# Kernel tuning notes

Measured on AMD Instinct MI355X. Metric: run time of the kernel, lower is better.

## Reference

```python
import jax, jax.numpy as jnp
import numpy as np

HEADS = 8
DIM_HEAD = 128
ATTN_MATRIX_SCALE = 1.5  # tau applied to mean-centered logits
SCALE = DIM_HEAD ** -0.5


def setup_inputs() -> dict:
    key = jax.random.key(0)
    ks = jax.random.split(key, 7)
    b, n, m = 2, 2048, 2048
    qd, cd, inner = 1024, 768, HEADS * DIM_HEAD
    x = jax.random.normal(ks[0], (b, n, qd), dtype=jnp.float32)
    context = jax.random.normal(ks[1], (b, m, cd), dtype=jnp.float32)
    Wq = jax.random.normal(ks[2], (qd, inner), dtype=jnp.float32) * (qd ** -0.5)
    Wk = jax.random.normal(ks[3], (cd, inner), dtype=jnp.float32) * (cd ** -0.5)
    Wv = jax.random.normal(ks[4], (cd, inner), dtype=jnp.float32) * (cd ** -0.5)
    Wout = jax.random.normal(ks[5], (inner, qd), dtype=jnp.float32) * (inner ** -0.5)
    bout = jnp.zeros((qd,), dtype=jnp.float32)
    return {"x": x, "context": context, "Wq": Wq, "Wk": Wk, "Wv": Wv,
            "Wout": Wout, "bout": bout}


def _split_heads(t):
    # (b, n, h*d) -> (h, b*n, d); matches rearrange '(b h) n d -> h (b n) d'
    b, n, _ = t.shape
    t = t.reshape(b, n, HEADS, DIM_HEAD)
    return t.transpose(2, 0, 1, 3).reshape(HEADS, b * n, DIM_HEAD)


def reference(x, context, Wq, Wk, Wv, Wout, bout):
    b, n, _ = x.shape
    qh = _split_heads(jnp.einsum('bnq,qi->bni', x, Wq))        # (h, b*n, d)
    kh = _split_heads(jnp.einsum('bmc,ci->bmi', context, Wk))  # (h, b*m, d)
    vh = _split_heads(jnp.einsum('bmc,ci->bmi', context, Wv))  # (h, b*m, d)

    # custom mean-centered / tau-scaled similarity (_compute_sim_with_tau)
    sim = jnp.einsum('hid,hjd->hij', qh, kh) * SCALE
    mean = jnp.mean(sim, axis=-1, keepdims=True)
    sim = (sim - mean) * ATTN_MATRIX_SCALE + mean

    attn = jax.nn.softmax(sim, axis=-1)
    out = jnp.einsum('hij,hjd->hid', attn, vh)                 # (h, b*n, d)

    # (h, b*n, d) -> (b, n, h*d)
    out = out.reshape(HEADS, b, n, DIM_HEAD).transpose(1, 2, 0, 3)
    out = out.reshape(b, n, HEADS * DIM_HEAD)
    return jnp.einsum('bni,iq->bnq', out, Wout) + bout
```

## Files before the change

kernel.cpp:

```cpp
#include <hip/hip_runtime.h>
#include <cstdint>
#include <cstddef>

typedef unsigned short u16t;
typedef __bf16 bf16x8_t __attribute__((ext_vector_type(8)));
typedef float f32x4_t __attribute__((ext_vector_type(4)));
typedef float f32x16_t __attribute__((ext_vector_type(16)));

#define MFMA_BF16 __builtin_amdgcn_mfma_f32_16x16x32_bf16
#define MFMA32    __builtin_amdgcn_mfma_f32_32x32x16_bf16

__device__ __forceinline__ u16t f2bf(float f) {
    uint32_t u = __builtin_bit_cast(uint32_t, f);
    u += 0x7fffu + ((u >> 16) & 1u);
    return (u16t)(u >> 16);
}

__device__ __forceinline__ uint32_t pk2bf(float a, float b) {
    return (uint32_t)f2bf(a) | ((uint32_t)f2bf(b) << 16);
}

__device__ __forceinline__ float bflo(uint32_t u) {
    return __builtin_bit_cast(float, u << 16);
}
__device__ __forceinline__ float bfhi(uint32_t u) {
    return __builtin_bit_cast(float, u & 0xffff0000u);
}

__device__ __forceinline__ bf16x8_t ld_frag(const u16t* p) {
    return __builtin_bit_cast(bf16x8_t, *(const uint4*)p);
}

__device__ __forceinline__ uint32_t cvtpk(float lo, float hi) {
    uint32_t r;
    asm("v_cvt_pk_bf16_f32 %0, %1, %2" : "=v"(r) : "v"(lo), "v"(hi));
    return r;
}
__device__ __forceinline__ void swap32(uint32_t& a, uint32_t& b) {
    asm("v_permlane32_swap_b32 %0, %1" : "+v"(a), "+v"(b));
}

__device__ __forceinline__ void gl_lds16(const u16t* g, u16t* l) {
    __builtin_amdgcn_global_load_lds(
        (const __attribute__((address_space(1))) void*)g,
        (__attribute__((address_space(3))) void*)l, 16, 0, 0);
}

__global__ void cast2_bf16_kernel(const float* __restrict__ s0, u16t* __restrict__ d0, int n0,
                                  const float* __restrict__ s1, u16t* __restrict__ d1, int n1) {
    int i = blockIdx.x * blockDim.x + threadIdx.x;
    const float* s; u16t* d;
    if (i < n0) { s = s0; d = d0; }
    else { i -= n0; if (i >= n1) return; s = s1; d = d1; }
    float4 v = ((const float4*)s)[i];
    uint2 o;
    o.x = pk2bf(v.x, v.y);
    o.y = pk2bf(v.z, v.w);
    ((uint2*)d)[i] = o;
}

__global__ void transpose4_kernel(const float* __restrict__ Wq, const float* __restrict__ Wk,
                                  const float* __restrict__ Wv, const float* __restrict__ Wo,
                                  u16t* __restrict__ Wqt, u16t* __restrict__ Wkt,
                                  u16t* __restrict__ Wvt, u16t* __restrict__ Wot) {
    const int z = blockIdx.z;
    const float* W = z == 0 ? Wq : (z == 1 ? Wk : (z == 2 ? Wv : Wo));
    u16t* Wt      = z == 0 ? Wqt : (z == 1 ? Wkt : (z == 2 ? Wvt : Wot));
    const int K   = (z == 1 || z == 2) ? 768 : 1024;
    const int N = 1024;
    int n0 = blockIdx.x * 32, k0 = blockIdx.y * 32;
    if (k0 >= K) return;
    __shared__ float tile[32][33];
    int tx = threadIdx.x, ty = threadIdx.y;
    for (int i = ty; i < 32; i += 8)
        tile[i][tx] = W[(size_t)(k0 + i) * N + n0 + tx];
    __syncthreads();
    for (int i = ty; i < 32; i += 8)
        Wt[(size_t)(n0 + i) * K + k0 + tx] = f2bf(tile[tx][i]);
}

__device__ __forceinline__ void gemm_core(
    const u16t* __restrict__ A, const u16t* __restrict__ Bt,
    int K, void* __restrict__ outp, const float* __restrict__ bias,
    int mode, float oscale, int bm, int bn)
{
    __shared__ __align__(16) u16t As[2][128 * 64];
    __shared__ __align__(16) u16t Bs[2][64 * 64];
    const int tid = threadIdx.x;
    const int wave = tid >> 6, lane = tid & 63;
    const int wm = wave & 1, wn = wave >> 1;
    const int quad = lane >> 4, l16 = lane & 15;

    const int l8r = lane >> 3, l8c = lane & 7;
    const int cgx = (l8c ^ l8r) * 8;

    f32x4_t acc[4][2];
#pragma unroll
    for (int i = 0; i < 4; ++i)
#pragma unroll
        for (int j = 0; j < 2; ++j) acc[i][j] = (f32x4_t){0.f, 0.f, 0.f, 0.f};

    const int nk = K >> 6;

#pragma unroll
    for (int it = 0; it < 4; ++it) {
        int rb = wave * 32 + it * 8;
        gl_lds16(&A[(size_t)(bm + rb + l8r) * K + cgx], &As[0][rb * 64]);
    }
#pragma unroll
    for (int it = 0; it < 2; ++it) {
        int rb = wave * 16 + it * 8;
        gl_lds16(&Bt[(size_t)(bn + rb + l8r) * K + cgx], &Bs[0][rb * 64]);
    }

    for (int ki = 0; ki < nk; ++ki) {
        const int buf = ki & 1;
        __syncthreads();

        if (ki + 1 < nk) {
            const int kc = (ki + 1) << 6;
#pragma unroll
            for (int it = 0; it < 4; ++it) {
                int rb = wave * 32 + it * 8;
                gl_lds16(&A[(size_t)(bm + rb + l8r) * K + kc + cgx], &As[buf ^ 1][rb * 64]);
            }
#pragma unroll
            for (int it = 0; it < 2; ++it) {
                int rb = wave * 16 + it * 8;
                gl_lds16(&Bt[(size_t)(bn + rb + l8r) * K + kc + cgx], &Bs[buf ^ 1][rb * 64]);
            }
        }

#pragma unroll
        for (int ks = 0; ks < 2; ++ks) {
            bf16x8_t af[4], bfv[2];
#pragma unroll
            for (int i = 0; i < 4; ++i) {
                int r = wm * 64 + i * 16 + l16;
                af[i] = ld_frag(&As[buf][r * 64 + (((ks * 4 + quad) ^ (r & 7)) * 8)]);
            }
#pragma unroll
            for (int j = 0; j < 2; ++j) {
                int r = wn * 32 + j * 16 + l16;
                bfv[j] = ld_frag(&Bs[buf][r * 64 + (((ks * 4 + quad) ^ (r & 7)) * 8)]);
            }
#pragma unroll
            for (int i = 0; i < 4; ++i)
#pragma unroll
                for (int j = 0; j < 2; ++j)
                    acc[i][j] = MFMA_BF16(af[i], bfv[j], acc[i][j], 0, 0, 0);
        }
    }

    if (mode == 3) {
        float* out = (float*)outp;
#pragma unroll
        for (int j = 0; j < 2; ++j) {
            int c = bn + wn * 32 + j * 16 + l16;
            float b = bias[c];
#pragma unroll
            for (int i = 0; i < 4; ++i) {
                int rb = bm + wm * 64 + i * 16 + quad * 4;
#pragma unroll
                for (int r = 0; r < 4; ++r)
                    out[(size_t)(rb + r) * 1024 + c] = acc[i][j][r] + b;
            }
        }
    } else if (mode == 2) {
        u16t* out = (u16t*)outp;
#pragma unroll
        for (int i = 0; i < 4; ++i)
#pragma unroll
            for (int j = 0; j < 2; ++j) {
                int rb = bm + wm * 64 + i * 16 + quad * 4;
                int c = bn + wn * 32 + j * 16 + l16;
                int h = c >> 7, d = c & 127;
                uint2 pk;
                pk.x = pk2bf(acc[i][j][0], acc[i][j][1]);
                pk.y = pk2bf(acc[i][j][2], acc[i][j][3]);
                *(uint2*)&out[((size_t)h * 128 + d) * 4096 + rb] = pk;
            }
    } else {
        u16t* out = (u16t*)outp;
#pragma unroll
        for (int i = 0; i < 4; ++i)
#pragma unroll
            for (int j = 0; j < 2; ++j) {
                int rb = bm + wm * 64 + i * 16 + quad * 4;
                int c = bn + wn * 32 + j * 16 + l16;
                int h = c >> 7, d = c & 127;
#pragma unroll
                for (int r = 0; r < 4; ++r)
                    out[((size_t)h * 4096 + rb + r) * 128 + d] = f2bf(acc[i][j][r] * oscale);
            }
    }
}

__global__ __launch_bounds__(256) void gemm_bf16_kernel(
    const u16t* __restrict__ A, const u16t* __restrict__ Bt,
    int K, void* __restrict__ outp, const float* __restrict__ bias,
    int mode, float oscale)
{
    gemm_core(A, Bt, K, outp, bias, mode, oscale, blockIdx.y * 128, blockIdx.x * 64);
}

__global__ __launch_bounds__(256) void qkv_kernel(
    const u16t* __restrict__ x_bf, const u16t* __restrict__ ctx_bf,
    const u16t* __restrict__ Wqt, const u16t* __restrict__ Wkt,
    const u16t* __restrict__ Wvt,
    u16t* __restrict__ Qh, u16t* __restrict__ Kh, u16t* __restrict__ Vt,
    float qscale)
{
    const int z = blockIdx.z;
    const u16t* A  = (z == 0) ? x_bf : ctx_bf;
    const u16t* Bt = (z == 0) ? Wqt : ((z == 1) ? Wkt : Wvt);
    void* outp     = (z == 0) ? (void*)Qh : ((z == 1) ? (void*)Kh : (void*)Vt);
    const int K    = (z == 0) ? 1024 : 768;
    const int mode = (z == 2) ? 2 : 0;
    const float sc = (z == 0) ? qscale : 1.0f;
    gemm_core(A, Bt, K, outp, nullptr, mode, sc, blockIdx.y * 128, blockIdx.x * 64);
}

__global__ __launch_bounds__(256, 2) void flash_kernel(
    const u16t* __restrict__ Qh, const u16t* __restrict__ Kh,
    const u16t* __restrict__ Vtg, u16t* __restrict__ Op0,
    u16t* __restrict__ Op1, float* __restrict__ lp)
{
    extern __shared__ __align__(16) u16t smem[];
    const int h = blockIdx.y;
    const int q0 = blockIdx.x * 128;
    const int z = blockIdx.z;
    const int tid = threadIdx.x;
    const int wave = tid >> 6, lane = tid & 63;
    const int l31 = lane & 31, hh = lane >> 5;
    const int NT = 64;

    const u16t* Kg = Kh + (size_t)h * 4096 * 128 + (size_t)z * 2048 * 128;
    const u16t* Vg = Vtg + (size_t)h * 128 * 4096 + z * 2048;

    {
        const u16t* Qg = Qh + ((size_t)h * 4096 + q0) * 128;
#pragma unroll
        for (int it = 0; it < 8; ++it) {
            int slot = it * 256 + tid;
            int r = slot >> 4, c = slot & 15;
            uint4 v = *(const uint4*)&Qg[(size_t)r * 128 + c * 8];
            *(uint4*)&smem[r * 128 + ((c ^ (r & 15)) * 8)] = v;
        }
    }
    __syncthreads();
    bf16x8_t qf[8];
    {
        int r = wave * 32 + l31;
#pragma unroll
        for (int s = 0; s < 8; ++s)
            qf[s] = ld_frag(&smem[r * 128 + (((s * 2 + hh) ^ (r & 15)) * 8)]);
    }
    __syncthreads();

    const bool kRole = wave < 2;
    const int wh = wave & 1;
    const int rK = lane >> 4, cK = lane & 15;
    const int rV = lane >> 2, cV = lane & 3;

    if (kRole) {
#pragma unroll
        for (int it = 0; it < 4; ++it) {
            int is = wh * 4 + it;
            int rowL = is * 4 + rK;
            gl_lds16(Kg + (size_t)rowL * 128 + ((cK ^ (rowL & 15)) * 8),
                     smem + is * 512);
        }
    } else {
#pragma unroll
        for (int it = 0; it < 4; ++it) {
            int is = wh * 4 + it;
            int rowL = is * 16 + rV;
            gl_lds16(Vg + (size_t)rowL * 4096 + ((cV ^ ((rowL >> 1) & 3)) * 8),
                     smem + 8192 + is * 512);
        }
    }

    f32x16_t Ow[4];
#pragma unroll
    for (int dg = 0; dg < 4; ++dg)
#pragma unroll
        for (int r = 0; r < 16; ++r) Ow[dg][r] = 0.f;

    float lsum = 0.f;
    const int swz = l31 & 15;
    bf16x8_t pf0, pf1;
    int v_rd = 2;
    int v_wr = 1;

    for (int t = 0; t <= NT; ++t) {
        __syncthreads();

        if (t + 1 < NT) {
            const int j0 = (t + 1) * 32;
            if (kRole) {
                u16t* kd = smem + ((t + 1) & 1) * 4096;
#pragma unroll
                for (int it = 0; it < 4; ++it) {
                    int is = wh * 4 + it;
                    int rowL = is * 4 + rK;
                    gl_lds16(Kg + (size_t)(j0 + rowL) * 128 + ((cK ^ (rowL & 15)) * 8),
                             kd + is * 512);
                }
            } else {
                u16t* vd = smem + 8192 + v_wr * 4096;
#pragma unroll
                for (int it = 0; it < 4; ++it) {
                    int is = wh * 4 + it;
                    int rowL = is * 16 + rV;
                    gl_lds16(Vg + (size_t)rowL * 4096 + j0 + ((cV ^ ((rowL >> 1) & 3)) * 8),
                             vd + is * 512);
                }
            }
        }

        if (t >= 1) {
            const u16t* vb = smem + 8192 + v_rd * 4096;
            __builtin_amdgcn_s_setprio(1);
#pragma unroll
            for (int dg = 0; dg < 4; ++dg) {
                int rv = dg * 32 + l31;
                int vsw = (rv >> 1) & 3;
                bf16x8_t v0 = ld_frag(&vb[rv * 32 + ((hh ^ vsw) * 8)]);
                bf16x8_t v1 = ld_frag(&vb[rv * 32 + (((2 + hh) ^ vsw) * 8)]);
                Ow[dg] = MFMA32(v0, pf0, Ow[dg], 0, 0, 0);
                Ow[dg] = MFMA32(v1, pf1, Ow[dg], 0, 0, 0);
            }
            __builtin_amdgcn_s_setprio(0);
        }

        if (t < NT) {
            const u16t* kb = smem + (t & 1) * 4096;
            f32x16_t Sa, Sb;
#pragma unroll
            for (int r = 0; r < 16; ++r) { Sa[r] = 0.f; Sb[r] = 0.f; }
            __builtin_amdgcn_s_setprio(1);
#pragma unroll
            for (int s = 0; s < 8; s += 2) {
                bf16x8_t k0 = ld_frag(&kb[l31 * 128 + (((s * 2 + hh) ^ swz) * 8)]);
                bf16x8_t k1 = ld_frag(&kb[l31 * 128 + ((((s + 1) * 2 + hh) ^ swz) * 8)]);
                Sa = MFMA32(k0, qf[s], Sa, 0, 0, 0);
                Sb = MFMA32(k1, qf[s + 1], Sb, 0, 0, 0);
            }
            __builtin_amdgcn_s_setprio(0);

            float p[16];
#pragma unroll
            for (int r = 0; r < 16; ++r)
                p[r] = __builtin_amdgcn_exp2f(Sa[r] + Sb[r]);
            lsum += ((((p[0] + p[1]) + (p[2] + p[3])) + ((p[4] + p[5]) + (p[6] + p[7])))
                  + (((p[8] + p[9]) + (p[10] + p[11])) + ((p[12] + p[13]) + (p[14] + p[15]))));

            uint32_t w0 = cvtpk(p[0], p[1]),   w2 = cvtpk(p[4], p[5]);
            uint32_t w1 = cvtpk(p[2], p[3]),   w3 = cvtpk(p[6], p[7]);
            swap32(w0, w2); swap32(w1, w3);
            uint32_t y0 = cvtpk(p[8], p[9]),   y2 = cvtpk(p[12], p[13]);
            uint32_t y1 = cvtpk(p[10], p[11]), y3 = cvtpk(p[14], p[15]);
            swap32(y0, y2); swap32(y1, y3);
            uint4 pw0; pw0.x = w0; pw0.y = w1; pw0.z = w2; pw0.w = w3;
            uint4 pw1; pw1.x = y0; pw1.y = y1; pw1.z = y2; pw1.w = y3;
            pf0 = __builtin_bit_cast(bf16x8_t, pw0);
            pf1 = __builtin_bit_cast(bf16x8_t, pw1);
        }

        v_rd = v_rd + 1 == 3 ? 0 : v_rd + 1;
        v_wr = v_wr + 1 == 3 ? 0 : v_wr + 1;
    }

    lsum += __shfl_xor(lsum, 32, 64);
    u16t* Op = z ? Op1 : Op0;
    size_t i = (size_t)(q0 + wave * 32 + l31);
    if (hh == 0) lp[z * 32768 + i * 8 + h] = lsum;
#pragma unroll
    for (int dg = 0; dg < 4; ++dg)
#pragma unroll
        for (int g = 0; g < 4; ++g) {
            uint2 pk;
            pk.x = pk2bf(Ow[dg][g * 4 + 0], Ow[dg][g * 4 + 1]);
            pk.y = pk2bf(Ow[dg][g * 4 + 2], Ow[dg][g * 4 + 3]);
            *(uint2*)&Op[i * 1024 + h * 128 + dg * 32 + g * 8 + hh * 4] = pk;
        }
}

__global__ __launch_bounds__(256) void combine_kernel(
    const u16t* __restrict__ O0, const u16t* __restrict__ O1,
    const float* __restrict__ lp, u16t* __restrict__ out)
{
    int t = blockIdx.x * blockDim.x + threadIdx.x;
    int e = t << 3;
    int i = e >> 10, h = (e >> 7) & 7;
    float inv = 1.f / (lp[i * 8 + h] + lp[32768 + i * 8 + h]);
    uint4 a = ((const uint4*)O0)[t];
    uint4 b = ((const uint4*)O1)[t];
    uint4 r;
    r.x = pk2bf((bflo(a.x) + bflo(b.x)) * inv, (bfhi(a.x) + bfhi(b.x)) * inv);
    r.y = pk2bf((bflo(a.y) + bflo(b.y)) * inv, (bfhi(a.y) + bfhi(b.y)) * inv);
    r.z = pk2bf((bflo(a.z) + bflo(b.z)) * inv, (bfhi(a.z) + bfhi(b.z)) * inv);
    r.w = pk2bf((bflo(a.w) + bflo(b.w)) * inv, (bfhi(a.w) + bfhi(b.w)) * inv);
    ((uint4*)out)[t] = r;
}

extern "C" void kernel_launch(void* const* d_in, const int* in_sizes, int n_in,
                              void* d_out, int out_size, void* d_ws, size_t ws_size,
                              hipStream_t stream)
{
    (void)in_sizes; (void)n_in; (void)out_size; (void)ws_size;
    const float* x    = (const float*)d_in[0];
    const float* ctx  = (const float*)d_in[1];
    const float* Wq   = (const float*)d_in[2];
    const float* Wk   = (const float*)d_in[3];
    const float* Wv   = (const float*)d_in[4];
    const float* Wout = (const float*)d_in[5];
    const float* bout = (const float*)d_in[6];
    float* out = (float*)d_out;

    u16t* ws = (u16t*)d_ws;
    u16t* x_bf   = ws;
    u16t* ctx_bf = x_bf + 4194304;
    u16t* Wqt    = ctx_bf + 3145728;
    u16t* Wkt    = Wqt + 1048576;
    u16t* Wvt    = Wkt + 786432;
    u16t* Woutt  = Wvt + 786432;
    u16t* Qh     = Woutt + 1048576;
    u16t* Kh     = Qh + 4194304;
    u16t* Vt     = Kh + 4194304;
    u16t* Oh   = x_bf;
    u16t* Ohp1 = ws + 4194304;
    float* lp  = (float*)(ws + 8388608);

    constexpr float QSCALE = 1.5f * 0.08838834764831845f * 1.4426950408889634f;

    (void)hipFuncSetAttribute((const void*)flash_kernel,
                              hipFuncAttributeMaxDynamicSharedMemorySize, 40960);

    cast2_bf16_kernel<<<7168, 256, 0, stream>>>(x, x_bf, 1048576, ctx, ctx_bf, 786432);
    transpose4_kernel<<<dim3(32, 32, 4), dim3(32, 8), 0, stream>>>(
        Wq, Wk, Wv, Wout, Wqt, Wkt, Wvt, Woutt);

    qkv_kernel<<<dim3(16, 32, 3), 256, 0, stream>>>(
        x_bf, ctx_bf, Wqt, Wkt, Wvt, Qh, Kh, Vt, QSCALE);

    flash_kernel<<<dim3(32, 8, 2), 256, 40960, stream>>>(Qh, Kh, Vt, Oh, Ohp1, lp);
    combine_kernel<<<2048, 256, 0, stream>>>(Oh, Ohp1, lp, Oh);

    gemm_bf16_kernel<<<dim3(16, 32), 256, 0, stream>>>(Oh, Woutt, 1024, out, bout, 3, 1.0f);
}
```

Baseline: 239.3 us.

## Load Q/K/V fragments directly from global into registers, dropping LDS staging

```diff
diff --git a/kernel.cpp b/kernel.cpp
--- a/kernel.cpp
+++ b/kernel.cpp
@@ -226,7 +226,6 @@
     const u16t* __restrict__ Vtg, u16t* __restrict__ Op0,
     u16t* __restrict__ Op1, float* __restrict__ lp)
 {
-    extern __shared__ __align__(16) u16t smem[];
     const int h = blockIdx.y;
     const int q0 = blockIdx.x * 128;
     const int z = blockIdx.z;
@@ -238,49 +237,21 @@
     const u16t* Kg = Kh + (size_t)h * 4096 * 128 + (size_t)z * 2048 * 128;
     const u16t* Vg = Vtg + (size_t)h * 128 * 4096 + z * 2048;
 
-    {
-        const u16t* Qg = Qh + ((size_t)h * 4096 + q0) * 128;
-#pragma unroll
-        for (int it = 0; it < 8; ++it) {
-            int slot = it * 256 + tid;
-            int r = slot >> 4, c = slot & 15;
-            uint4 v = *(const uint4*)&Qg[(size_t)r * 128 + c * 8];
-            *(uint4*)&smem[r * 128 + ((c ^ (r & 15)) * 8)] = v;
-        }
-    }
-    __syncthreads();
     bf16x8_t qf[8];
     {
-        int r = wave * 32 + l31;
-#pragma unroll
-        for (int s = 0; s < 8; ++s)
-            qf[s] = ld_frag(&smem[r * 128 + (((s * 2 + hh) ^ (r & 15)) * 8)]);
-    }
-    __syncthreads();
-
-    const bool kRole = wave < 2;
-    const int wh = wave & 1;
-    const int rK = lane >> 4, cK = lane & 15;
-    const int rV = lane >> 2, cV = lane & 3;
-
-    if (kRole) {
-#pragma unroll
-        for (int it = 0; it < 4; ++it) {
-            int is = wh * 4 + it;
-            int rowL = is * 4 + rK;
-            gl_lds16(Kg + (size_t)rowL * 128 + ((cK ^ (rowL & 15)) * 8),
-                     smem + is * 512);
-        }
-    } else {
-#pragma unroll
-        for (int it = 0; it < 4; ++it) {
-            int is = wh * 4 + it;
-            int rowL = is * 16 + rV;
-            gl_lds16(Vg + (size_t)rowL * 4096 + ((cV ^ ((rowL >> 1) & 3)) * 8),
-                     smem + 8192 + is * 512);
-        }
-    }
-
+        const u16t* Qr = Qh + ((size_t)h * 4096 + q0 + wave * 32 + l31) * 128 + hh * 8;
+#pragma unroll
+        for (int s = 0; s < 8; ++s) qf[s] = ld_frag(Qr + s * 16);
+    }
+
+    const u16t* Kr0 = Kg + (size_t)l31 * 128 + hh * 8;
+    const u16t* Vr0 = Vg + (size_t)l31 * 4096 + hh * 8;
+
+    bf16x8_t kf[8];
+#pragma unroll
+    for (int s = 0; s < 8; ++s) kf[s] = ld_frag(Kr0 + s * 16);
+
+    bf16x8_t vf0[4], vf1[4];
     f32x16_t Ow[4];
 #pragma unroll
     for (int dg = 0; dg < 4; ++dg)
@@ -288,88 +259,65 @@
         for (int r = 0; r < 16; ++r) Ow[dg][r] = 0.f;
 
     float lsum = 0.f;
-    const int swz = l31 & 15;
     bf16x8_t pf0, pf1;
-    int v_rd = 2;
-    int v_wr = 1;
-
-    for (int t = 0; t <= NT; ++t) {
-        __syncthreads();
+
+    for (int t = 0; t < NT; ++t) {
+        f32x16_t Sa, Sb;
+#pragma unroll
+        for (int r = 0; r < 16; ++r) { Sa[r] = 0.f; Sb[r] = 0.f; }
+        __builtin_amdgcn_s_setprio(1);
+#pragma unroll
+        for (int s = 0; s < 8; s += 2) {
+            Sa = MFMA32(kf[s], qf[s], Sa, 0, 0, 0);
+            Sb = MFMA32(kf[s + 1], qf[s + 1], Sb, 0, 0, 0);
+        }
+        if (t >= 1) {
+#pragma unroll
+            for (int dg = 0; dg < 4; ++dg) {
+                Ow[dg] = MFMA32(vf0[dg], pf0, Ow[dg], 0, 0, 0);
+                Ow[dg] = MFMA32(vf1[dg], pf1, Ow[dg], 0, 0, 0);
+            }
+        }
+        __builtin_amdgcn_s_setprio(0);
 
         if (t + 1 < NT) {
-            const int j0 = (t + 1) * 32;
-            if (kRole) {
-                u16t* kd = smem + ((t + 1) & 1) * 4096;
-#pragma unroll
-                for (int it = 0; it < 4; ++it) {
-                    int is = wh * 4 + it;
-                    int rowL = is * 4 + rK;
-                    gl_lds16(Kg + (size_t)(j0 + rowL) * 128 + ((cK ^ (rowL & 15)) * 8),
-                             kd + is * 512);
-                }
-            } else {
-                u16t* vd = smem + 8192 + v_wr * 4096;
-#pragma unroll
-                for (int it = 0; it < 4; ++it) {
-                    int is = wh * 4 + it;
-                    int rowL = is * 16 + rV;
-                    gl_lds16(Vg + (size_t)rowL * 4096 + j0 + ((cV ^ ((rowL >> 1) & 3)) * 8),
-                             vd + is * 512);
-                }
-            }
-        }
-
-        if (t >= 1) {
-            const u16t* vb = smem + 8192 + v_rd * 4096;
-            __builtin_amdgcn_s_setprio(1);
+            const u16t* Kr = Kr0 + (size_t)(t + 1) * 4096;
+#pragma unroll
+            for (int s = 0; s < 8; ++s) kf[s] = ld_frag(Kr + s * 16);
+        }
+        {
+            const u16t* Vr = Vr0 + t * 32;
 #pragma unroll
             for (int dg = 0; dg < 4; ++dg) {
-                int rv = dg * 32 + l31;
-                int vsw = (rv >> 1) & 3;
-                bf16x8_t v0 = ld_frag(&vb[rv * 32 + ((hh ^ vsw) * 8)]);
-                bf16x8_t v1 = ld_frag(&vb[rv * 32 + (((2 + hh) ^ vsw) * 8)]);
-                Ow[dg] = MFMA32(v0, pf0, Ow[dg], 0, 0, 0);
-                Ow[dg] = MFMA32(v1, pf1, Ow[dg], 0, 0, 0);
-            }
-            __builtin_amdgcn_s_setprio(0);
-        }
-
-        if (t < NT) {
-            const u16t* kb = smem + (t & 1) * 4096;
-            f32x16_t Sa, Sb;
-#pragma unroll
-            for (int r = 0; r < 16; ++r) { Sa[r] = 0.f; Sb[r] = 0.f; }
-            __builtin_amdgcn_s_setprio(1);
-#pragma unroll
-            for (int s = 0; s < 8; s += 2) {
-                bf16x8_t k0 = ld_frag(&kb[l31 * 128 + (((s * 2 + hh) ^ swz) * 8)]);
-                bf16x8_t k1 = ld_frag(&kb[l31 * 128 + ((((s + 1) * 2 + hh) ^ swz) * 8)]);
-                Sa = MFMA32(k0, qf[s], Sa, 0, 0, 0);
-                Sb = MFMA32(k1, qf[s + 1], Sb, 0, 0, 0);
-            }
-            __builtin_amdgcn_s_setprio(0);
-
-            float p[16];
-#pragma unroll
-            for (int r = 0; r < 16; ++r)
-                p[r] = __builtin_amdgcn_exp2f(Sa[r] + Sb[r]);
-            lsum += ((((p[0] + p[1]) + (p[2] + p[3])) + ((p[4] + p[5]) + (p[6] + p[7])))
-                  + (((p[8] + p[9]) + (p[10] + p[11])) + ((p[12] + p[13]) + (p[14] + p[15]))));
-
-            uint32_t w0 = cvtpk(p[0], p[1]),   w2 = cvtpk(p[4], p[5]);
-            uint32_t w1 = cvtpk(p[2], p[3]),   w3 = cvtpk(p[6], p[7]);
-            swap32(w0, w2); swap32(w1, w3);
-            uint32_t y0 = cvtpk(p[8], p[9]),   y2 = cvtpk(p[12], p[13]);
-            uint32_t y1 = cvtpk(p[10], p[11]), y3 = cvtpk(p[14], p[15]);
-            swap32(y0, y2); swap32(y1, y3);
-            uint4 pw0; pw0.x = w0; pw0.y = w1; pw0.z = w2; pw0.w = w3;
-            uint4 pw1; pw1.x = y0; pw1.y = y1; pw1.z = y2; pw1.w = y3;
-            pf0 = __builtin_bit_cast(bf16x8_t, pw0);
-            pf1 = __builtin_bit_cast(bf16x8_t, pw1);
-        }
-
-        v_rd = v_rd + 1 == 3 ? 0 : v_rd + 1;
-        v_wr = v_wr + 1 == 3 ? 0 : v_wr + 1;
+                const u16t* vrp = Vr + (size_t)dg * 32 * 4096;
+                vf0[dg] = ld_frag(vrp);
+                vf1[dg] = ld_frag(vrp + 16);
+            }
+        }
+
+        float p[16];
+#pragma unroll
+        for (int r = 0; r < 16; ++r)
+            p[r] = __builtin_amdgcn_exp2f(Sa[r] + Sb[r]);
+        lsum += ((((p[0] + p[1]) + (p[2] + p[3])) + ((p[4] + p[5]) + (p[6] + p[7])))
+              + (((p[8] + p[9]) + (p[10] + p[11])) + ((p[12] + p[13]) + (p[14] + p[15]))));
+
+        uint32_t w0 = cvtpk(p[0], p[1]),   w2 = cvtpk(p[4], p[5]);
+        uint32_t w1 = cvtpk(p[2], p[3]),   w3 = cvtpk(p[6], p[7]);
+        swap32(w0, w2); swap32(w1, w3);
+        uint32_t y0 = cvtpk(p[8], p[9]),   y2 = cvtpk(p[12], p[13]);
+        uint32_t y1 = cvtpk(p[10], p[11]), y3 = cvtpk(p[14], p[15]);
+        swap32(y0, y2); swap32(y1, y3);
+        uint4 pw0; pw0.x = w0; pw0.y = w1; pw0.z = w2; pw0.w = w3;
+        uint4 pw1; pw1.x = y0; pw1.y = y1; pw1.z = y2; pw1.w = y3;
+        pf0 = __builtin_bit_cast(bf16x8_t, pw0);
+        pf1 = __builtin_bit_cast(bf16x8_t, pw1);
+    }
+
+#pragma unroll
+    for (int dg = 0; dg < 4; ++dg) {
+        Ow[dg] = MFMA32(vf0[dg], pf0, Ow[dg], 0, 0, 0);
+        Ow[dg] = MFMA32(vf1[dg], pf1, Ow[dg], 0, 0, 0);
     }
 
     lsum += __shfl_xor(lsum, 32, 64);
@@ -435,9 +383,6 @@
 
     constexpr float QSCALE = 1.5f * 0.08838834764831845f * 1.4426950408889634f;
 
-    (void)hipFuncSetAttribute((const void*)flash_kernel,
-                              hipFuncAttributeMaxDynamicSharedMemorySize, 40960);
-
     cast2_bf16_kernel<<<7168, 256, 0, stream>>>(x, x_bf, 1048576, ctx, ctx_bf, 786432);
     transpose4_kernel<<<dim3(32, 32, 4), dim3(32, 8), 0, stream>>>(
         Wq, Wk, Wv, Wout, Wqt, Wkt, Wvt, Woutt);
@@ -445,7 +390,7 @@
     qkv_kernel<<<dim3(16, 32, 3), 256, 0, stream>>>(
         x_bf, ctx_bf, Wqt, Wkt, Wvt, Qh, Kh, Vt, QSCALE);
 
-    flash_kernel<<<dim3(32, 8, 2), 256, 40960, stream>>>(Qh, Kh, Vt, Oh, Ohp1, lp);
+    flash_kernel<<<dim3(32, 8, 2), 256, 0, stream>>>(Qh, Kh, Vt, Oh, Ohp1, lp);
     combine_kernel<<<2048, 256, 0, stream>>>(Oh, Ohp1, lp, Oh);
 
     gemm_bf16_kernel<<<dim3(16, 32), 256, 0, stream>>>(Oh, Woutt, 1024, out, bout, 3, 1.0f);
```

Result: slower. 392.5 us (+64.0%).

## Double KV tile to 64 keys and restructure flash pipeline buffers

Applied to the files above, without the earlier changes.

```diff
diff --git a/kernel.cpp b/kernel.cpp
--- a/kernel.cpp
+++ b/kernel.cpp
@@ -233,7 +233,7 @@
     const int tid = threadIdx.x;
     const int wave = tid >> 6, lane = tid & 63;
     const int l31 = lane & 31, hh = lane >> 5;
-    const int NT = 64;
+    const int NT = 32;
 
     const u16t* Kg = Kh + (size_t)h * 4096 * 128 + (size_t)z * 2048 * 128;
     const u16t* Vg = Vtg + (size_t)h * 128 * 4096 + z * 2048;
@@ -261,24 +261,16 @@
     const bool kRole = wave < 2;
     const int wh = wave & 1;
     const int rK = lane >> 4, cK = lane & 15;
-    const int rV = lane >> 2, cV = lane & 3;
+    const int rV = lane >> 3, cV = lane & 7;
 
     if (kRole) {
 #pragma unroll
-        for (int it = 0; it < 4; ++it) {
-            int is = wh * 4 + it;
+        for (int it = 0; it < 8; ++it) {
+            int is = wh * 8 + it;
             int rowL = is * 4 + rK;
             gl_lds16(Kg + (size_t)rowL * 128 + ((cK ^ (rowL & 15)) * 8),
                      smem + is * 512);
         }
-    } else {
-#pragma unroll
-        for (int it = 0; it < 4; ++it) {
-            int is = wh * 4 + it;
-            int rowL = is * 16 + rV;
-            gl_lds16(Vg + (size_t)rowL * 4096 + ((cV ^ ((rowL >> 1) & 3)) * 8),
-                     smem + 8192 + is * 512);
-        }
     }
 
     f32x16_t Ow[4];
@@ -288,88 +280,89 @@
         for (int r = 0; r < 16; ++r) Ow[dg][r] = 0.f;
 
     float lsum = 0.f;
-    const int swz = l31 & 15;
-    bf16x8_t pf0, pf1;
-    int v_rd = 2;
-    int v_wr = 1;
+    const int swzk = l31 & 15;
+    bf16x8_t pf[4];
 
     for (int t = 0; t <= NT; ++t) {
         __syncthreads();
 
-        if (t + 1 < NT) {
-            const int j0 = (t + 1) * 32;
-            if (kRole) {
-                u16t* kd = smem + ((t + 1) & 1) * 4096;
-#pragma unroll
-                for (int it = 0; it < 4; ++it) {
-                    int is = wh * 4 + it;
+        if (kRole) {
+            if (t + 1 < NT) {
+                const int j0 = (t + 1) * 64;
+                u16t* kd = smem + ((t + 1) & 1) * 8192;
+#pragma unroll
+                for (int it = 0; it < 8; ++it) {
+                    int is = wh * 8 + it;
                     int rowL = is * 4 + rK;
                     gl_lds16(Kg + (size_t)(j0 + rowL) * 128 + ((cK ^ (rowL & 15)) * 8),
                              kd + is * 512);
                 }
-            } else {
-                u16t* vd = smem + 8192 + v_wr * 4096;
-#pragma unroll
-                for (int it = 0; it < 4; ++it) {
-                    int is = wh * 4 + it;
-                    int rowL = is * 16 + rV;
-                    gl_lds16(Vg + (size_t)rowL * 4096 + j0 + ((cV ^ ((rowL >> 1) & 3)) * 8),
+            }
+        } else {
+            if (t < NT) {
+                const int j0 = t * 64;
+                u16t* vd = smem + 16384 + (t & 1) * 8192;
+#pragma unroll
+                for (int it = 0; it < 8; ++it) {
+                    int is = wh * 8 + it;
+                    int rowL = is * 8 + rV;
+                    gl_lds16(Vg + (size_t)rowL * 4096 + j0 + ((cV ^ ((rowL ^ (rowL >> 3)) & 7)) * 8),
                              vd + is * 512);
                 }
             }
         }
 
+        __builtin_amdgcn_s_setprio(1);
+        f32x16_t St0, St1;
+#pragma unroll
+        for (int r = 0; r < 16; ++r) { St0[r] = 0.f; St1[r] = 0.f; }
+        if (t < NT) {
+            const u16t* kb = smem + (t & 1) * 8192;
+#pragma unroll
+            for (int s = 0; s < 8; ++s) {
+                int ch = ((s * 2 + hh) ^ swzk) * 8;
+                bf16x8_t k0 = ld_frag(&kb[l31 * 128 + ch]);
+                bf16x8_t k1 = ld_frag(&kb[(32 + l31) * 128 + ch]);
+                St0 = MFMA32(k0, qf[s], St0, 0, 0, 0);
+                St1 = MFMA32(k1, qf[s], St1, 0, 0, 0);
+            }
+        }
         if (t >= 1) {
-            const u16t* vb = smem + 8192 + v_rd * 4096;
-            __builtin_amdgcn_s_setprio(1);
+            const u16t* vb = smem + 16384 + ((t - 1) & 1) * 8192;
 #pragma unroll
             for (int dg = 0; dg < 4; ++dg) {
                 int rv = dg * 32 + l31;
-                int vsw = (rv >> 1) & 3;
-                bf16x8_t v0 = ld_frag(&vb[rv * 32 + ((hh ^ vsw) * 8)]);
-                bf16x8_t v1 = ld_frag(&vb[rv * 32 + (((2 + hh) ^ vsw) * 8)]);
-                Ow[dg] = MFMA32(v0, pf0, Ow[dg], 0, 0, 0);
-                Ow[dg] = MFMA32(v1, pf1, Ow[dg], 0, 0, 0);
-            }
-            __builtin_amdgcn_s_setprio(0);
-        }
+                int gsw = (rv ^ (rv >> 3)) & 7;
+#pragma unroll
+                for (int sl = 0; sl < 4; ++sl) {
+                    bf16x8_t vf = ld_frag(&vb[rv * 64 + (((sl * 2 + hh) ^ gsw) * 8)]);
+                    Ow[dg] = MFMA32(vf, pf[sl], Ow[dg], 0, 0, 0);
+                }
+            }
+        }
+        __builtin_amdgcn_s_setprio(0);
 
         if (t < NT) {
-            const u16t* kb = smem + (t & 1) * 4096;
-            f32x16_t Sa, Sb;
-#pragma unroll
-            for (int r = 0; r < 16; ++r) { Sa[r] = 0.f; Sb[r] = 0.f; }
-            __builtin_amdgcn_s_setprio(1);
-#pragma unroll
-            for (int s = 0; s < 8; s += 2) {
-                bf16x8_t k0 = ld_frag(&kb[l31 * 128 + (((s * 2 + hh) ^ swz) * 8)]);
-                bf16x8_t k1 = ld_frag(&kb[l31 * 128 + ((((s + 1) * 2 + hh) ^ swz) * 8)]);
-                Sa = MFMA32(k0, qf[s], Sa, 0, 0, 0);
-                Sb = MFMA32(k1, qf[s + 1], Sb, 0, 0, 0);
-            }
-            __builtin_amdgcn_s_setprio(0);
-
-            float p[16];
-#pragma unroll
-            for (int r = 0; r < 16; ++r)
-                p[r] = __builtin_amdgcn_exp2f(Sa[r] + Sb[r]);
-            lsum += ((((p[0] + p[1]) + (p[2] + p[3])) + ((p[4] + p[5]) + (p[6] + p[7])))
-                  + (((p[8] + p[9]) + (p[10] + p[11])) + ((p[12] + p[13]) + (p[14] + p[15]))));
-
-            uint32_t w0 = cvtpk(p[0], p[1]),   w2 = cvtpk(p[4], p[5]);
-            uint32_t w1 = cvtpk(p[2], p[3]),   w3 = cvtpk(p[6], p[7]);
-            swap32(w0, w2); swap32(w1, w3);
-            uint32_t y0 = cvtpk(p[8], p[9]),   y2 = cvtpk(p[12], p[13]);
-            uint32_t y1 = cvtpk(p[10], p[11]), y3 = cvtpk(p[14], p[15]);
-            swap32(y0, y2); swap32(y1, y3);
-            uint4 pw0; pw0.x = w0; pw0.y = w1; pw0.z = w2; pw0.w = w3;
-            uint4 pw1; pw1.x = y0; pw1.y = y1; pw1.z = y2; pw1.w = y3;
-            pf0 = __builtin_bit_cast(bf16x8_t, pw0);
-            pf1 = __builtin_bit_cast(bf16x8_t, pw1);
-        }
-
-        v_rd = v_rd + 1 == 3 ? 0 : v_rd + 1;
-        v_wr = v_wr + 1 == 3 ? 0 : v_wr + 1;
+#pragma unroll
+            for (int half = 0; half < 2; ++half) {
+                float p[16];
+#pragma unroll
+                for (int r = 0; r < 16; ++r)
+                    p[r] = __builtin_amdgcn_exp2f(half ? St1[r] : St0[r]);
+                lsum += ((((p[0] + p[1]) + (p[2] + p[3])) + ((p[4] + p[5]) + (p[6] + p[7])))
+                      + (((p[8] + p[9]) + (p[10] + p[11])) + ((p[12] + p[13]) + (p[14] + p[15]))));
+                uint32_t w0 = cvtpk(p[0], p[1]),   w2 = cvtpk(p[4], p[5]);
+                uint32_t w1 = cvtpk(p[2], p[3]),   w3 = cvtpk(p[6], p[7]);
+                swap32(w0, w2); swap32(w1, w3);
+                uint32_t y0 = cvtpk(p[8], p[9]),   y2 = cvtpk(p[12], p[13]);
+                uint32_t y1 = cvtpk(p[10], p[11]), y3 = cvtpk(p[14], p[15]);
+                swap32(y0, y2); swap32(y1, y3);
+                uint4 pw0; pw0.x = w0; pw0.y = w1; pw0.z = w2; pw0.w = w3;
+                uint4 pw1; pw1.x = y0; pw1.y = y1; pw1.z = y2; pw1.w = y3;
+                pf[half * 2 + 0] = __builtin_bit_cast(bf16x8_t, pw0);
+                pf[half * 2 + 1] = __builtin_bit_cast(bf16x8_t, pw1);
+            }
+        }
     }
 
     lsum += __shfl_xor(lsum, 32, 64);
@@ -436,7 +429,7 @@
     constexpr float QSCALE = 1.5f * 0.08838834764831845f * 1.4426950408889634f;
 
     (void)hipFuncSetAttribute((const void*)flash_kernel,
-                              hipFuncAttributeMaxDynamicSharedMemorySize, 40960);
+                              hipFuncAttributeMaxDynamicSharedMemorySize, 65536);
 
     cast2_bf16_kernel<<<7168, 256, 0, stream>>>(x, x_bf, 1048576, ctx, ctx_bf, 786432);
     transpose4_kernel<<<dim3(32, 32, 4), dim3(32, 8), 0, stream>>>(
@@ -445,7 +438,7 @@
     qkv_kernel<<<dim3(16, 32, 3), 256, 0, stream>>>(
         x_bf, ctx_bf, Wqt, Wkt, Wvt, Qh, Kh, Vt, QSCALE);
 
-    flash_kernel<<<dim3(32, 8, 2), 256, 40960, stream>>>(Qh, Kh, Vt, Oh, Ohp1, lp);
+    flash_kernel<<<dim3(32, 8, 2), 256, 65536, stream>>>(Qh, Kh, Vt, Oh, Ohp1, lp);
     combine_kernel<<<2048, 256, 0, stream>>>(Oh, Ohp1, lp, Oh);
 
     gemm_bf16_kernel<<<dim3(16, 32), 256, 0, stream>>>(Oh, Woutt, 1024, out, bout, 3, 1.0f);
```

Result: faster. 234.6 us (-2.0%).
